# Optimization experiments

Hardware: AMD Instinct MI355X
Metric: run time of the kernel (lower is better)

The kernel has to match this reference:

```python
import jax, jax.numpy as jnp
import numpy as np

B, S, D, H = 4, 512, 768, 200


def setup_inputs() -> dict:
    key = jax.random.key(0)
    ks = jax.random.split(key, 6)
    x = jax.random.normal(ks[0], (B, S, D), dtype=jnp.float32)
    # Linear default init ~ U(-1/sqrt(fan_in), 1/sqrt(fan_in)); scaled normal is fine for a baseline
    W_head = jax.random.normal(ks[1], (D, H), dtype=jnp.float32) * (1.0 / np.sqrt(D))
    b_head = jnp.zeros((H,), dtype=jnp.float32)
    W_tail = jax.random.normal(ks[2], (D, H), dtype=jnp.float32) * (1.0 / np.sqrt(D))
    b_tail = jnp.zeros((H,), dtype=jnp.float32)
    # xavier_normal on [200,200,200]: fan_in = fan_out = 200*200 -> std = sqrt(2/80000)
    U = jax.random.normal(ks[3], (H, H, H), dtype=jnp.float32) * np.sqrt(2.0 / (2 * H * H))
    W_down = jax.random.normal(ks[4], (H, 1), dtype=jnp.float32) * (1.0 / np.sqrt(H))
    b_down = jnp.zeros((1,), dtype=jnp.float32)
    return {"x": x, "W_head": W_head, "b_head": b_head, "W_tail": W_tail,
            "b_tail": b_tail, "U": U, "W_down": W_down, "b_down": b_down}


def reference(x, W_head, b_head, W_tail, b_tail, U, W_down, b_down):
    # head/tail projections with ReLU: [B,S,H]
    head = jax.nn.relu(x @ W_head + b_head)
    tail = jax.nn.relu(x @ W_tail + b_tail)
    # biaffine: 'bxi,oij,byj->bxyo' done as two contractions
    tmp = jnp.einsum('bxi,oij->bxoj', head, U)            # [B,S,H,H]
    logits = jnp.einsum('bxoj,byj->bxyo', tmp, tail)       # [B,S,S,H] (== permuted boxy)
    # down_layer(200->1).squeeze(-1); rope branch in source is dead (rope_logits = 0)
    scores = (logits @ W_down)[..., 0] + b_down[0]         # [B,S,S]
    return scores / jnp.sqrt(jnp.asarray(200.0, dtype=scores.dtype))
```

## Files before the change

### kernel.cpp

```cpp
#include <hip/hip_runtime.h>

#define H 200
#define D 768
#define BATCH 4
#define S 512
#define M (BATCH*S)
#define KP 224
#define NP 208
#define NCAT 400
#define NC4 (H*H/4)
#define VT_BLOCKS 313
#define PREP_BLOCKS 1000

typedef __attribute__((ext_vector_type(8))) short bf16x8;
typedef __attribute__((ext_vector_type(4))) float f32x4;
typedef unsigned short us;

__device__ inline us f2bf(float f) {
    union { float f; unsigned u; } v; v.f = f;
    return (us)((v.u + 0x7FFF + ((v.u >> 16) & 1)) >> 16);
}

__global__ __launch_bounds__(256) void prep(
        const float* __restrict__ x,  const float* __restrict__ Wh,
        const float* __restrict__ Wt, const float* __restrict__ U,
        const float* __restrict__ Wd,
        us* __restrict__ xb, us* __restrict__ Wcb, us* __restrict__ VTb,
        us* __restrict__ headb, us* __restrict__ tailb, us* __restrict__ hvb) {
    int bid = blockIdx.x;
    if (bid < VT_BLOCKS) {
        __shared__ float4 red[8][32];
        int cl = threadIdx.x & 31, q = threadIdx.x >> 5;
        int c = bid * 32 + cl;
        const float4* U4 = (const float4*)U;
        float4 acc = make_float4(0.f, 0.f, 0.f, 0.f);
        if (c < NC4) {
            int o0 = q * 25;
            #pragma unroll
            for (int o = o0; o < o0 + 25; ++o) {
                float w = Wd[o];
                float4 u = U4[(size_t)o * NC4 + c];
                acc.x += w * u.x; acc.y += w * u.y;
                acc.z += w * u.z; acc.w += w * u.w;
            }
        }
        red[q][cl] = acc;
        __syncthreads();
        if (q == 0 && c < NC4) {
            #pragma unroll
            for (int g = 1; g < 8; ++g) {
                float4 r = red[g][cl];
                acc.x += r.x; acc.y += r.y; acc.z += r.z; acc.w += r.w;
            }
            int i = c / (H / 4), j0 = (c % (H / 4)) * 4;
            VTb[(j0 + 0) * KP + i] = f2bf(acc.x);
            VTb[(j0 + 1) * KP + i] = f2bf(acc.y);
            VTb[(j0 + 2) * KP + i] = f2bf(acc.z);
            VTb[(j0 + 3) * KP + i] = f2bf(acc.w);
        }
        return;
    }
    const int GTH = (PREP_BLOCKS - VT_BLOCKS) * 256;
    int gtid = (bid - VT_BLOCKS) * 256 + threadIdx.x;
    {
        const float4* x4 = (const float4*)x;
        ushort4* xb4 = (ushort4*)xb;
        for (int t = gtid; t < M * D / 4; t += GTH) {
            float4 v = x4[t];
            ushort4 o; o.x = f2bf(v.x); o.y = f2bf(v.y); o.z = f2bf(v.z); o.w = f2bf(v.w);
            xb4[t] = o;
        }
    }
    for (int id = gtid; id < NCAT * D; id += GTH) {
        int n = id / D, k = id % D;
        float v = (n < H) ? Wh[k * H + n] : Wt[k * H + (n - H)];
        Wcb[id] = f2bf(v);
    }
    for (int id = gtid; id < M * (KP - H); id += GTH) {
        int r = id / (KP - H), c = H + id % (KP - H);
        headb[r * KP + c] = 0; tailb[r * KP + c] = 0;
    }
    for (int id = gtid; id < M * (KP - NP); id += GTH) {
        int r = id / (KP - NP), c = NP + id % (KP - NP);
        hvb[r * KP + c] = 0;
    }
    for (int id = gtid; id < H * (KP - H); id += GTH) {
        int n = id / (KP - H), k = H + id % (KP - H);
        VTb[n * KP + k] = 0;
    }
    for (int id = gtid; id < (NP - H) * KP; id += GTH) {
        int n = H + id / KP, k = id % KP;
        VTb[n * KP + k] = 0;
    }
}

__global__ __launch_bounds__(64) void proj_mfma(
        const us* __restrict__ xb, const us* __restrict__ Wcb,
        const float* __restrict__ bh, const float* __restrict__ bt,
        us* __restrict__ headb, us* __restrict__ tailb) {
    int lane = threadIdx.x, quad = lane >> 4, col = lane & 15;
    int m0 = blockIdx.x * 32, n0 = blockIdx.y * 16;
    const bf16x8* A0 = (const bf16x8*)(xb + (m0 + col) * D + quad * 8);
    const bf16x8* A1 = (const bf16x8*)(xb + (m0 + 16 + col) * D + quad * 8);
    const bf16x8* Bp = (const bf16x8*)(Wcb + (n0 + col) * D + quad * 8);
    f32x4 acc0 = {0.f,0.f,0.f,0.f}, acc1 = {0.f,0.f,0.f,0.f};
    #pragma unroll 4
    for (int kk = 0; kk < D / 32; ++kk) {
        bf16x8 a0 = A0[kk * 4];
        bf16x8 a1 = A1[kk * 4];
        bf16x8 b  = Bp[kk * 4];
        acc0 = __builtin_amdgcn_mfma_f32_16x16x32_bf16(a0, b, acc0, 0, 0, 0);
        acc1 = __builtin_amdgcn_mfma_f32_16x16x32_bf16(a1, b, acc1, 0, 0, 0);
    }
    int n = n0 + col;
    bool ish = (n < H);
    float bias = ish ? bh[n] : bt[n - H];
    us* dst = ish ? headb : tailb;
    int nn = ish ? n : n - H;
    #pragma unroll
    for (int r = 0; r < 4; ++r) {
        int ma = m0 + quad * 4 + r;
        dst[ma * KP + nn]        = f2bf(fmaxf(acc0[r] + bias, 0.f));
        dst[(ma + 16) * KP + nn] = f2bf(fmaxf(acc1[r] + bias, 0.f));
    }
}

__global__ __launch_bounds__(64) void hv_mfma(
        const us* __restrict__ headb, const us* __restrict__ VTb,
        us* __restrict__ hvb) {
    int lane = threadIdx.x, quad = lane >> 4, col = lane & 15;
    int m0 = blockIdx.x * 32, n0 = blockIdx.y * 16;
    const bf16x8* A0 = (const bf16x8*)(headb + (m0 + col) * KP + quad * 8);
    const bf16x8* A1 = (const bf16x8*)(headb + (m0 + 16 + col) * KP + quad * 8);
    const bf16x8* Bp = (const bf16x8*)(VTb + (n0 + col) * KP + quad * 8);
    f32x4 acc0 = {0.f,0.f,0.f,0.f}, acc1 = {0.f,0.f,0.f,0.f};
    #pragma unroll
    for (int kk = 0; kk < KP / 32; ++kk) {
        bf16x8 a0 = A0[kk * 4];
        bf16x8 a1 = A1[kk * 4];
        bf16x8 b  = Bp[kk * 4];
        acc0 = __builtin_amdgcn_mfma_f32_16x16x32_bf16(a0, b, acc0, 0, 0, 0);
        acc1 = __builtin_amdgcn_mfma_f32_16x16x32_bf16(a1, b, acc1, 0, 0, 0);
    }
    int n = n0 + col;
    #pragma unroll
    for (int r = 0; r < 4; ++r) {
        int ma = m0 + quad * 4 + r;
        hvb[ma * KP + n]        = f2bf(acc0[r]);
        hvb[(ma + 16) * KP + n] = f2bf(acc1[r]);
    }
}

__global__ __launch_bounds__(64) void scores_mfma(
        const us* __restrict__ hvb, const us* __restrict__ tailb,
        const float* __restrict__ bd, float* __restrict__ out) {
    int lane = threadIdx.x, quad = lane >> 4, col = lane & 15;
    int b = blockIdx.z;
    int m0 = blockIdx.x * 32, n0 = blockIdx.y * 32;
    const us* A  = hvb   + (size_t)b * S * KP;
    const us* Bm = tailb + (size_t)b * S * KP;
    const bf16x8* A0 = (const bf16x8*)(A  + (m0 + col) * KP + quad * 8);
    const bf16x8* A1 = (const bf16x8*)(A  + (m0 + 16 + col) * KP + quad * 8);
    const bf16x8* B0 = (const bf16x8*)(Bm + (n0 + col) * KP + quad * 8);
    const bf16x8* B1 = (const bf16x8*)(Bm + (n0 + 16 + col) * KP + quad * 8);
    f32x4 a00 = {0.f,0.f,0.f,0.f}, a01 = {0.f,0.f,0.f,0.f};
    f32x4 a10 = {0.f,0.f,0.f,0.f}, a11 = {0.f,0.f,0.f,0.f};
    #pragma unroll
    for (int kk = 0; kk < KP / 32; ++kk) {
        bf16x8 a0 = A0[kk * 4];
        bf16x8 a1 = A1[kk * 4];
        bf16x8 b0 = B0[kk * 4];
        bf16x8 b1 = B1[kk * 4];
        a00 = __builtin_amdgcn_mfma_f32_16x16x32_bf16(a0, b0, a00, 0, 0, 0);
        a01 = __builtin_amdgcn_mfma_f32_16x16x32_bf16(a0, b1, a01, 0, 0, 0);
        a10 = __builtin_amdgcn_mfma_f32_16x16x32_bf16(a1, b0, a10, 0, 0, 0);
        a11 = __builtin_amdgcn_mfma_f32_16x16x32_bf16(a1, b1, a11, 0, 0, 0);
    }
    float bias = bd[0];
    const float scale = 0.07071067811865475f;
    float* outb = out + (size_t)b * S * S;
    #pragma unroll
    for (int r = 0; r < 4; ++r) {
        int ma = m0 + quad * 4 + r, mb = ma + 16;
        outb[ma * S + n0 + col]      = (a00[r] + bias) * scale;
        outb[ma * S + n0 + 16 + col] = (a01[r] + bias) * scale;
        outb[mb * S + n0 + col]      = (a10[r] + bias) * scale;
        outb[mb * S + n0 + 16 + col] = (a11[r] + bias) * scale;
    }
}

extern "C" void kernel_launch(void* const* d_in, const int* in_sizes, int n_in,
                              void* d_out, int out_size, void* d_ws, size_t ws_size,
                              hipStream_t stream) {
    const float* x  = (const float*)d_in[0];
    const float* Wh = (const float*)d_in[1];
    const float* bh = (const float*)d_in[2];
    const float* Wt = (const float*)d_in[3];
    const float* bt = (const float*)d_in[4];
    const float* U  = (const float*)d_in[5];
    const float* Wd = (const float*)d_in[6];
    const float* bd = (const float*)d_in[7];
    float* out = (float*)d_out;

    us* xb    = (us*)d_ws;
    us* Wcb   = xb    + (size_t)M * D;
    us* VTb   = Wcb   + (size_t)NCAT * D;
    us* hvb   = VTb   + (size_t)NP * KP;
    us* headb = hvb   + (size_t)M * KP;
    us* tailb = headb + (size_t)M * KP;

    prep<<<PREP_BLOCKS, 256, 0, stream>>>(x, Wh, Wt, U, Wd,
                                          xb, Wcb, VTb, headb, tailb, hvb);
    proj_mfma<<<dim3(M / 32, NCAT / 16), 64, 0, stream>>>(xb, Wcb, bh, bt, headb, tailb);
    hv_mfma<<<dim3(M / 32, NP / 16), 64, 0, stream>>>(headb, VTb, hvb);
    scores_mfma<<<dim3(S / 32, S / 32, BATCH), 64, 0, stream>>>(hvb, tailb, bd, out);
}
```

Before: 119.1 us.

## Move U·Wd reduction into projection kernel so it overlaps the MFMA GEMM

The prep kernel now only converts x and the projection weights to bf16. The U·Wd reduction (VT), the head/tail projection MFMA tiles and the padding zero-fill are combined into one heterogeneous launch with block-range dispatch, and projection tiles are packed four waves per 256-thread block. This is meant to overlap the bandwidth-heavy 32 MB read of U with the compute-bound projection GEMM and to save a launch. In exchange, VT blocks and GEMM blocks now compete for the same CUs, and the xb conversion still has to finish before the combined kernel starts.

```diff
diff --git a/kernel.cpp b/kernel.cpp
--- a/kernel.cpp
+++ b/kernel.cpp
@@ -10,7 +10,10 @@
 #define NCAT 400
 #define NC4 (H*H/4)
 #define VT_BLOCKS 313
-#define PREP_BLOCKS 1000
+#define PROJ_BLOCKS 400
+#define PAD_BLOCKS 32
+#define K2_BLOCKS (VT_BLOCKS + PROJ_BLOCKS + PAD_BLOCKS)
+#define PREP_BLOCKS 512
 
 typedef __attribute__((ext_vector_type(8))) short bf16x8;
 typedef __attribute__((ext_vector_type(4))) float f32x4;
@@ -21,12 +24,34 @@
     return (us)((v.u + 0x7FFF + ((v.u >> 16) & 1)) >> 16);
 }
 
-__global__ __launch_bounds__(256) void prep(
+__global__ __launch_bounds__(256) void prep_lite(
         const float* __restrict__ x,  const float* __restrict__ Wh,
-        const float* __restrict__ Wt, const float* __restrict__ U,
-        const float* __restrict__ Wd,
-        us* __restrict__ xb, us* __restrict__ Wcb, us* __restrict__ VTb,
-        us* __restrict__ headb, us* __restrict__ tailb, us* __restrict__ hvb) {
+        const float* __restrict__ Wt,
+        us* __restrict__ xb, us* __restrict__ Wcb) {
+    const int GTH = PREP_BLOCKS * 256;
+    int gtid = blockIdx.x * 256 + threadIdx.x;
+    {
+        const float4* x4 = (const float4*)x;
+        ushort4* xb4 = (ushort4*)xb;
+        for (int t = gtid; t < M * D / 4; t += GTH) {
+            float4 v = x4[t];
+            ushort4 o; o.x = f2bf(v.x); o.y = f2bf(v.y); o.z = f2bf(v.z); o.w = f2bf(v.w);
+            xb4[t] = o;
+        }
+    }
+    for (int id = gtid; id < NCAT * D; id += GTH) {
+        int n = id / D, k = id % D;
+        float v = (n < H) ? Wh[k * H + n] : Wt[k * H + (n - H)];
+        Wcb[id] = f2bf(v);
+    }
+}
+
+__global__ __launch_bounds__(256) void projvt(
+        const float* __restrict__ U,  const float* __restrict__ Wd,
+        const us* __restrict__ xb,    const us* __restrict__ Wcb,
+        const float* __restrict__ bh, const float* __restrict__ bt,
+        us* __restrict__ VTb, us* __restrict__ headb, us* __restrict__ tailb,
+        us* __restrict__ hvb) {
     int bid = blockIdx.x;
     if (bid < VT_BLOCKS) {
         __shared__ float4 red[8][32];
@@ -60,22 +85,40 @@
         }
         return;
     }
-    const int GTH = (PREP_BLOCKS - VT_BLOCKS) * 256;
-    int gtid = (bid - VT_BLOCKS) * 256 + threadIdx.x;
-    {
-        const float4* x4 = (const float4*)x;
-        ushort4* xb4 = (ushort4*)xb;
-        for (int t = gtid; t < M * D / 4; t += GTH) {
-            float4 v = x4[t];
-            ushort4 o; o.x = f2bf(v.x); o.y = f2bf(v.y); o.z = f2bf(v.z); o.w = f2bf(v.w);
-            xb4[t] = o;
-        }
-    }
-    for (int id = gtid; id < NCAT * D; id += GTH) {
-        int n = id / D, k = id % D;
-        float v = (n < H) ? Wh[k * H + n] : Wt[k * H + (n - H)];
-        Wcb[id] = f2bf(v);
-    }
+    bid -= VT_BLOCKS;
+    if (bid < PROJ_BLOCKS) {
+        int w = threadIdx.x >> 6, lane = threadIdx.x & 63;
+        int t = bid * 4 + w;
+        int quad = lane >> 4, col = lane & 15;
+        int m0 = (t & 63) * 32, n0 = (t >> 6) * 16;
+        const bf16x8* A0 = (const bf16x8*)(xb + (m0 + col) * D + quad * 8);
+        const bf16x8* A1 = (const bf16x8*)(xb + (m0 + 16 + col) * D + quad * 8);
+        const bf16x8* Bp = (const bf16x8*)(Wcb + (n0 + col) * D + quad * 8);
+        f32x4 acc0 = {0.f,0.f,0.f,0.f}, acc1 = {0.f,0.f,0.f,0.f};
+        #pragma unroll 4
+        for (int kk = 0; kk < D / 32; ++kk) {
+            bf16x8 a0 = A0[kk * 4];
+            bf16x8 a1 = A1[kk * 4];
+            bf16x8 b  = Bp[kk * 4];
+            acc0 = __builtin_amdgcn_mfma_f32_16x16x32_bf16(a0, b, acc0, 0, 0, 0);
+            acc1 = __builtin_amdgcn_mfma_f32_16x16x32_bf16(a1, b, acc1, 0, 0, 0);
+        }
+        int n = n0 + col;
+        bool ish = (n < H);
+        float bias = ish ? bh[n] : bt[n - H];
+        us* dst = ish ? headb : tailb;
+        int nn = ish ? n : n - H;
+        #pragma unroll
+        for (int r = 0; r < 4; ++r) {
+            int ma = m0 + quad * 4 + r;
+            dst[ma * KP + nn]        = f2bf(fmaxf(acc0[r] + bias, 0.f));
+            dst[(ma + 16) * KP + nn] = f2bf(fmaxf(acc1[r] + bias, 0.f));
+        }
+        return;
+    }
+    bid -= PROJ_BLOCKS;
+    const int GTH = PAD_BLOCKS * 256;
+    int gtid = bid * 256 + threadIdx.x;
     for (int id = gtid; id < M * (KP - H); id += GTH) {
         int r = id / (KP - H), c = H + id % (KP - H);
         headb[r * KP + c] = 0; tailb[r * KP + c] = 0;
@@ -91,37 +134,6 @@
     for (int id = gtid; id < (NP - H) * KP; id += GTH) {
         int n = H + id / KP, k = id % KP;
         VTb[n * KP + k] = 0;
-    }
-}
-
-__global__ __launch_bounds__(64) void proj_mfma(
-        const us* __restrict__ xb, const us* __restrict__ Wcb,
-        const float* __restrict__ bh, const float* __restrict__ bt,
-        us* __restrict__ headb, us* __restrict__ tailb) {
-    int lane = threadIdx.x, quad = lane >> 4, col = lane & 15;
-    int m0 = blockIdx.x * 32, n0 = blockIdx.y * 16;
-    const bf16x8* A0 = (const bf16x8*)(xb + (m0 + col) * D + quad * 8);
-    const bf16x8* A1 = (const bf16x8*)(xb + (m0 + 16 + col) * D + quad * 8);
-    const bf16x8* Bp = (const bf16x8*)(Wcb + (n0 + col) * D + quad * 8);
-    f32x4 acc0 = {0.f,0.f,0.f,0.f}, acc1 = {0.f,0.f,0.f,0.f};
-    #pragma unroll 4
-    for (int kk = 0; kk < D / 32; ++kk) {
-        bf16x8 a0 = A0[kk * 4];
-        bf16x8 a1 = A1[kk * 4];
-        bf16x8 b  = Bp[kk * 4];
-        acc0 = __builtin_amdgcn_mfma_f32_16x16x32_bf16(a0, b, acc0, 0, 0, 0);
-        acc1 = __builtin_amdgcn_mfma_f32_16x16x32_bf16(a1, b, acc1, 0, 0, 0);
-    }
-    int n = n0 + col;
-    bool ish = (n < H);
-    float bias = ish ? bh[n] : bt[n - H];
-    us* dst = ish ? headb : tailb;
-    int nn = ish ? n : n - H;
-    #pragma unroll
-    for (int r = 0; r < 4; ++r) {
-        int ma = m0 + quad * 4 + r;
-        dst[ma * KP + nn]        = f2bf(fmaxf(acc0[r] + bias, 0.f));
-        dst[(ma + 16) * KP + nn] = f2bf(fmaxf(acc1[r] + bias, 0.f));
     }
 }
 
@@ -209,9 +221,9 @@
     us* headb = hvb   + (size_t)M * KP;
     us* tailb = headb + (size_t)M * KP;
 
-    prep<<<PREP_BLOCKS, 256, 0, stream>>>(x, Wh, Wt, U, Wd,
-                                          xb, Wcb, VTb, headb, tailb, hvb);
-    proj_mfma<<<dim3(M / 32, NCAT / 16), 64, 0, stream>>>(xb, Wcb, bh, bt, headb, tailb);
+    prep_lite<<<PREP_BLOCKS, 256, 0, stream>>>(x, Wh, Wt, xb, Wcb);
+    projvt<<<K2_BLOCKS, 256, 0, stream>>>(U, Wd, xb, Wcb, bh, bt,
+                                          VTb, headb, tailb, hvb);
     hv_mfma<<<dim3(M / 32, NP / 16), 64, 0, stream>>>(headb, VTb, hvb);
     scores_mfma<<<dim3(S / 32, S / 32, BATCH), 64, 0, stream>>>(hvb, tailb, bd, out);
 }
```

Result: no change. 117.2 us (median of 2 runs) (-1.5%).
